# Performance work log

Hardware: AMD Instinct MI355X
Metric: run time of the kernel (lower is better)

Reference implementation:

```python
import jax, jax.numpy as jnp
import numpy as np

N, NODE_IN, EDGE_IN, H, ROUNDS = 768, 64, 32, 128, 2


def setup_inputs() -> dict:
    key = jax.random.key(0)
    ks = jax.random.split(key, 12)
    node_feats = jax.random.normal(ks[0], (N, NODE_IN), dtype=jnp.float32)
    edge_feats = jax.random.normal(ks[1], (N, N, EDGE_IN), dtype=jnp.float32)
    adj_mask = jax.random.randint(ks[2], (N, N), 0, 2).astype(jnp.float32)
    def lin(k, fan_in, fan_out):
        w = jax.random.normal(k, (fan_in, fan_out), dtype=jnp.float32) / jnp.sqrt(fan_in)
        return w
    return {
        "node_feats": node_feats,
        "edge_feats": edge_feats,
        "adj_mask": adj_mask,
        "Wn": lin(ks[3], NODE_IN, H), "bn": jnp.zeros((H,), jnp.float32),
        "We": lin(ks[4], EDGE_IN, H), "be": jnp.zeros((H,), jnp.float32),
        "Wa": lin(ks[5], 2 * H, H), "ba": jnp.zeros((H,), jnp.float32),
        "Wu": lin(ks[6], 2 * H, H), "bu": jnp.zeros((H,), jnp.float32),
    }


def reference(node_feats, edge_feats, adj_mask, Wn, bn, We, be, Wa, ba, Wu, bu):
    relu = jax.nn.relu
    h = relu(node_feats @ Wn + bn)                      # (N, H)
    e = relu(jnp.einsum('ijf,fk->ijk', edge_feats, We) + be)  # (N, N, H)
    deg = jnp.clip(adj_mask.sum(axis=0), 1.0)[:, None]  # (N, 1) receiver degree
    # Precompute edge contribution to agg_lin once (constant across rounds):
    # concat([sender, e]) @ Wa == sender @ Wa[:H] + e @ Wa[H:]
    e_proj = jnp.einsum('ijh,hk->ijk', e, Wa[H:])       # (N, N, H)
    for _ in range(ROUNDS):
        s_proj = h @ Wa[:H]                              # (N, H) sender part
        msgs = relu(s_proj[:, None, :] + e_proj + ba)    # (N, N, H)
        agg = jnp.einsum('ijk,ij->jk', msgs, adj_mask) / deg  # masked sum over senders i
        h = relu(jnp.concatenate([h, agg], axis=-1) @ Wu + bu)
    graph_emb = h.mean(axis=0)
    return (h, graph_emb)
```

## Files before the change

### kernel.cpp

```cpp
#include <hip/hip_runtime.h>
#include <hip/hip_bf16.h>


typedef __bf16 bf16x8 __attribute__((ext_vector_type(8)));
typedef float f32x4 __attribute__((ext_vector_type(4)));

#define NN 768

static __device__ __forceinline__ unsigned short to_bf16u(float x) {
    return __builtin_bit_cast(unsigned short, (__bf16)x);
}

__global__ __launch_bounds__(256) void k_prep(
                       const float* __restrict__ adj, float* __restrict__ adjT,
                       const float* __restrict__ We, const float* __restrict__ Wa,
                       unsigned short* __restrict__ WeT, unsigned short* __restrict__ Wa2T,
                       const float* __restrict__ nf, const float* __restrict__ Wn,
                       const float* __restrict__ bn, const float* __restrict__ ba,
                       float* __restrict__ h, float* __restrict__ sp) {
    const int b = blockIdx.x, tid = threadIdx.x;
    if (b < 576) {
        __shared__ float tile[32][33];
        int bx = b % 24, by = b / 24;
        int tx = tid & 31, ty = tid >> 5;
#pragma unroll
        for (int yy = 0; yy < 32; yy += 8)
            tile[ty + yy][tx] = adj[(size_t)(by * 32 + ty + yy) * NN + bx * 32 + tx];
        __syncthreads();
#pragma unroll
        for (int yy = 0; yy < 32; yy += 8)
            adjT[(size_t)(bx * 32 + ty + yy) * NN + by * 32 + tx] = tile[tx][ty + yy];
    } else if (b < 656) {
        int g = (b - 576) * 256 + tid;
        if (g < 128 * 32) {
            int c = g >> 5, f = g & 31;
            WeT[g] = to_bf16u(We[f * 128 + c]);
        } else {
            int g2 = g - 128 * 32;
            int c = g2 >> 7, k = g2 & 127;
            Wa2T[g2] = to_bf16u(Wa[(128 + k) * 128 + c]);
        }
    } else if (b < 1040) {
        __shared__ float nf_l[2][64];
        __shared__ float h_l[2][128];
        int row = tid >> 7, t = tid & 127;
        int i = (b - 656) * 2 + row;
        if (t < 64) nf_l[row][t] = nf[i * 64 + t];
        __syncthreads();
        float acc = bn[t];
#pragma unroll 8
        for (int f = 0; f < 64; ++f) acc += nf_l[row][f] * Wn[f * 128 + t];
        acc = fmaxf(acc, 0.f);
        h[i * 128 + t] = acc;
        h_l[row][t] = acc;
        __syncthreads();
        float spv = ba[t];
#pragma unroll 8
        for (int f = 0; f < 128; ++f) spv += h_l[row][f] * Wa[f * 128 + t];
        sp[i * 128 + t] = spv;
    } else {
        if (tid < 128) sp[(size_t)NN * 128 + tid] = -1e30f;
    }
}

__global__ __launch_bounds__(512) void k_big(
    const float* __restrict__ ef, const float* __restrict__ adjT,
    const float* __restrict__ sp, const unsigned short* __restrict__ WeT,
    const unsigned short* __restrict__ Wa2T, const float* __restrict__ be,
    float* __restrict__ agg) {
    __shared__ __align__(16) unsigned short e_lds[2][2][16 * 128];
    __shared__ unsigned short idx_lds[NN];
    __shared__ float be_lds[128];
    __shared__ int s_cnt;
    __shared__ float s_invdeg;

    const int tid  = threadIdx.x;
    const int j    = blockIdx.x;
    const int lane = tid & 63;
    const int wv   = tid >> 6;
    const int wr   = wv >> 2;
    const int wc   = wv & 3;
    const int lg   = lane >> 4;
    const int lr   = lane & 15;

    if (tid < 128) be_lds[tid] = be[tid];

    bf16x8 bwe[2];
    bf16x8 bwa[2][4];
#pragma unroll
    for (int t = 0; t < 2; ++t) {
        const int col = 32 * wc + 16 * t + lr;
        bwe[t] = *reinterpret_cast<const bf16x8*>(WeT + col * 32 + 8 * lg);
#pragma unroll
        for (int s = 0; s < 4; ++s)
            bwa[t][s] = *reinterpret_cast<const bf16x8*>(Wa2T + col * 128 + 32 * s + 8 * lg);
    }

    if (wv == 0) {
        int cnt = 0;
#pragma unroll
        for (int b = 0; b < 12; ++b) {
            float v = adjT[(size_t)j * NN + b * 64 + lane];
            unsigned long long m = __ballot(v != 0.0f);
            if (v != 0.0f) {
                int pos = cnt + __popcll(m & ((1ULL << lane) - 1ULL));
                idx_lds[pos] = (unsigned short)(b * 64 + lane);
            }
            cnt += (int)__popcll(m);
        }
        if (lane == 0) {
            s_cnt = cnt;
            s_invdeg = 1.0f / fmaxf((float)cnt, 1.0f);
        }
    }
    __syncthreads();

    const int cnt = s_cnt;
    const int Kc = (cnt + 31) >> 5;

    float aggp[2] = {0.f, 0.f};

    auto load_ef = [&](int m, float4& x0, float4& x1) {
        int s = 32 * m + 16 * wr + lr;
        int r = (s < cnt) ? (int)idx_lds[s] : 0;
        const float* p = ef + ((size_t)r * NN + j) * 32 + 8 * lg;
        x0 = *reinterpret_cast<const float4*>(p);
        x1 = *reinterpret_cast<const float4*>(p + 4);
    };
    auto gemm1 = [&](const float4& x0, const float4& x1, int buf) {
        bf16x8 a;
        a[0] = (__bf16)x0.x; a[1] = (__bf16)x0.y; a[2] = (__bf16)x0.z; a[3] = (__bf16)x0.w;
        a[4] = (__bf16)x1.x; a[5] = (__bf16)x1.y; a[6] = (__bf16)x1.z; a[7] = (__bf16)x1.w;
#pragma unroll
        for (int t = 0; t < 2; ++t) {
            const int col = 32 * wc + 16 * t + lr;
            float bb = be_lds[col];
            f32x4 c;
            c[0] = bb; c[1] = bb; c[2] = bb; c[3] = bb;
            f32x4 C1 = __builtin_amdgcn_mfma_f32_16x16x32_bf16(a, bwe[t], c, 0, 0, 0);
#pragma unroll
            for (int r = 0; r < 4; ++r) {
                int row = 4 * lg + r;
                int idx = (row * 128 + col) ^ ((row & 7) << 3);
                e_lds[buf][wr][idx] = to_bf16u(fmaxf(C1[r], 0.f));
            }
        }
    };

    float4 c0, c1;
    if (Kc > 0) {
        load_ef(0, c0, c1);
        gemm1(c0, c1, 0);
        if (Kc > 1) load_ef(1, c0, c1);
    }
    __syncthreads();

    for (int n = 0; n < Kc; ++n) {
        const int b = n & 1;
        float4 p0, p1;
        if (n + 2 < Kc) load_ef(n + 2, p0, p1);
        if (n + 1 < Kc) gemm1(c0, c1, b ^ 1);

        bf16x8 ae[4];
#pragma unroll
        for (int s = 0; s < 4; ++s) {
            int idx = (lr * 128 + 32 * s + 8 * lg) ^ ((lr & 7) << 3);
            ae[s] = *reinterpret_cast<const bf16x8*>(&e_lds[b][wr][idx]);
        }
        int srow[4];
#pragma unroll
        for (int r = 0; r < 4; ++r) {
            int s = 32 * n + 16 * wr + 4 * lg + r;
            srow[r] = (s < cnt) ? (int)idx_lds[s] : NN;
        }
#pragma unroll
        for (int t = 0; t < 2; ++t) {
            const int col = 32 * wc + 16 * t + lr;
            f32x4 acc;
#pragma unroll
            for (int r = 0; r < 4; ++r)
                acc[r] = sp[(size_t)srow[r] * 128 + col];
#pragma unroll
            for (int s = 0; s < 4; ++s)
                acc = __builtin_amdgcn_mfma_f32_16x16x32_bf16(ae[s], bwa[t][s], acc, 0, 0, 0);
#pragma unroll
            for (int r = 0; r < 4; ++r)
                aggp[t] += fmaxf(acc[r], 0.f);
        }

        if (n + 2 < Kc) { c0 = p0; c1 = p1; }
        __syncthreads();
    }

    float* red = reinterpret_cast<float*>(&e_lds[0][0][0]);
#pragma unroll
    for (int t = 0; t < 2; ++t) {
        float v = aggp[t];
        v += __shfl_xor(v, 16);
        v += __shfl_xor(v, 32);
        if (lane < 16) red[wv * 32 + 16 * t + lane] = v;
    }
    __syncthreads();
    if (tid < 128) {
        int wcol = tid >> 5, c32 = tid & 31;
        agg[(size_t)j * 128 + tid] =
            (red[wcol * 32 + c32] + red[(4 + wcol) * 32 + c32]) * s_invdeg;
    }
}

template <int LAST>
__global__ __launch_bounds__(256) void k_upd(
                      const float* __restrict__ h_in, const float* __restrict__ agg,
                      const float* __restrict__ Wu, const float* __restrict__ bu,
                      const float* __restrict__ Wa, const float* __restrict__ ba,
                      float* __restrict__ h_out, float* __restrict__ sp,
                      float* __restrict__ out) {
    __shared__ float buf[2][256];
    __shared__ float hn[2][128];
    const int tid = threadIdx.x;
    const int row = tid >> 7, t = tid & 127;
    const int i = blockIdx.x * 2 + row;
    buf[row][t] = h_in[i * 128 + t];
    buf[row][128 + t] = agg[i * 128 + t];
    __syncthreads();
    float acc = bu[t];
#pragma unroll 8
    for (int f = 0; f < 256; ++f) acc += buf[row][f] * Wu[f * 128 + t];
    acc = fmaxf(acc, 0.f);
    if (LAST) {
        out[i * 128 + t] = acc;
    } else {
        h_out[i * 128 + t] = acc;
        hn[row][t] = acc;
        __syncthreads();
        float spv = ba[t];
#pragma unroll 8
        for (int f = 0; f < 128; ++f) spv += hn[row][f] * Wa[f * 128 + t];
        sp[i * 128 + t] = spv;
    }
}

__global__ __launch_bounds__(64) void k_gemb(const float* __restrict__ out_h, float* __restrict__ out) {
    int c = blockIdx.x, l = threadIdx.x;
    float acc = 0.f;
    for (int i = l; i < NN; i += 64) acc += out_h[(size_t)i * 128 + c];
#pragma unroll
    for (int off = 32; off; off >>= 1) acc += __shfl_down(acc, off);
    if (l == 0) out[NN * 128 + c] = acc * (1.0f / 768.0f);
}

extern "C" void kernel_launch(void* const* d_in, const int* in_sizes, int n_in,
                              void* d_out, int out_size, void* d_ws, size_t ws_size,
                              hipStream_t stream) {
    const float* nf  = (const float*)d_in[0];
    const float* ef  = (const float*)d_in[1];
    const float* adj = (const float*)d_in[2];
    const float* Wn  = (const float*)d_in[3];
    const float* bn  = (const float*)d_in[4];
    const float* We  = (const float*)d_in[5];
    const float* be  = (const float*)d_in[6];
    const float* Wa  = (const float*)d_in[7];
    const float* ba  = (const float*)d_in[8];
    const float* Wu  = (const float*)d_in[9];
    const float* bu  = (const float*)d_in[10];
    float* out = (float*)d_out;

    float* h_buf = (float*)d_ws;
    float* agg   = h_buf + NN * 128;
    float* sp    = agg + NN * 128;
    float* adjT  = sp + (NN + 1) * 128;
    unsigned short* WeT  = (unsigned short*)(adjT + NN * NN);
    unsigned short* Wa2T = WeT + 128 * 32;

    k_prep<<<1041, 256, 0, stream>>>(adj, adjT, We, Wa, WeT, Wa2T, nf, Wn, bn, ba, h_buf, sp);

    k_big<<<NN, 512, 0, stream>>>(ef, adjT, sp, WeT, Wa2T, be, agg);
    k_upd<0><<<NN / 2, 256, 0, stream>>>(h_buf, agg, Wu, bu, Wa, ba, h_buf, sp, out);
    k_big<<<NN, 512, 0, stream>>>(ef, adjT, sp, WeT, Wa2T, be, agg);
    k_upd<1><<<NN / 2, 256, 0, stream>>>(h_buf, agg, Wu, bu, Wa, ba, h_buf, sp, out);

    k_gemb<<<128, 64, 0, stream>>>(out, out);
}
```

Measured before the change: 146.0 us.

## Pre-transpose edge features to bf16 receiver-major layout for gather kernel

Adds a transpose kernel that converts edge features to bf16 laid out as [receiver][sender][feature]. A new aggregation kernel then reads contiguous, half-size rows per receiver in both rounds. The aim is to cut the strided fp32 gather traffic in the message kernel. The cost is an extra full pass over the edge tensor plus a large workspace write. The new path is used only when the workspace is big enough.

```diff
diff --git a/kernel.cpp b/kernel.cpp
--- a/kernel.cpp
+++ b/kernel.cpp
@@ -60,6 +60,171 @@
         sp[i * 128 + t] = spv;
     } else {
         if (tid < 128) sp[(size_t)NN * 128 + tid] = -1e30f;
+    }
+}
+
+__global__ __launch_bounds__(256) void k_eft(const float* __restrict__ ef,
+                                             unsigned short* __restrict__ efT) {
+    __shared__ unsigned short tile[8 * 1288 + 8];
+    const int b = blockIdx.x, t = threadIdx.x;
+    const int i0 = (b % 24) * 32, j0 = (b / 24) * 8;
+    {
+        const int jj = t >> 5, ff = t & 31;
+#pragma unroll 4
+        for (int i = 0; i < 32; ++i) {
+            float v = ef[((size_t)(i0 + i) * NN + j0 + jj) * 32 + ff];
+            tile[jj * 1288 + i * 40 + ff] = to_bf16u(v);
+        }
+    }
+    __syncthreads();
+    const int tp = t & 31, j = t >> 5;
+    unsigned short* dst = efT + ((size_t)(j0 + j) * NN + i0) * 32;
+#pragma unroll
+    for (int v = 0; v < 4; ++v) {
+        int flat = v * 256 + tp * 8;
+        int i = flat >> 5, f = flat & 31;
+        bf16x8 val = *reinterpret_cast<const bf16x8*>(&tile[j * 1288 + i * 40 + f]);
+        *reinterpret_cast<bf16x8*>(dst + flat) = val;
+    }
+}
+
+__global__ __launch_bounds__(512) void k_big_t(
+    const unsigned short* __restrict__ efT, const float* __restrict__ adjT,
+    const float* __restrict__ sp, const unsigned short* __restrict__ WeT,
+    const unsigned short* __restrict__ Wa2T, const float* __restrict__ be,
+    float* __restrict__ agg) {
+    __shared__ __align__(16) unsigned short e_lds[2][2][16 * 128];
+    __shared__ unsigned short idx_lds[NN];
+    __shared__ float be_lds[128];
+    __shared__ int s_cnt;
+    __shared__ float s_invdeg;
+
+    const int tid  = threadIdx.x;
+    const int j    = blockIdx.x;
+    const int lane = tid & 63;
+    const int wv   = tid >> 6;
+    const int wr   = wv >> 2;
+    const int wc   = wv & 3;
+    const int lg   = lane >> 4;
+    const int lr   = lane & 15;
+
+    if (tid < 128) be_lds[tid] = be[tid];
+
+    bf16x8 bwe[2];
+    bf16x8 bwa[2][4];
+#pragma unroll
+    for (int t = 0; t < 2; ++t) {
+        const int col = 32 * wc + 16 * t + lr;
+        bwe[t] = *reinterpret_cast<const bf16x8*>(WeT + col * 32 + 8 * lg);
+#pragma unroll
+        for (int s = 0; s < 4; ++s)
+            bwa[t][s] = *reinterpret_cast<const bf16x8*>(Wa2T + col * 128 + 32 * s + 8 * lg);
+    }
+
+    if (wv == 0) {
+        int cnt = 0;
+#pragma unroll
+        for (int b = 0; b < 12; ++b) {
+            float v = adjT[(size_t)j * NN + b * 64 + lane];
+            unsigned long long m = __ballot(v != 0.0f);
+            if (v != 0.0f) {
+                int pos = cnt + __popcll(m & ((1ULL << lane) - 1ULL));
+                idx_lds[pos] = (unsigned short)(b * 64 + lane);
+            }
+            cnt += (int)__popcll(m);
+        }
+        if (lane == 0) {
+            s_cnt = cnt;
+            s_invdeg = 1.0f / fmaxf((float)cnt, 1.0f);
+        }
+    }
+    __syncthreads();
+
+    const int cnt = s_cnt;
+    const int Kc = (cnt + 31) >> 5;
+
+    float aggp[2] = {0.f, 0.f};
+
+    auto load_ef = [&](int m, bf16x8& x) {
+        int s = 32 * m + 16 * wr + lr;
+        int r = (s < cnt) ? (int)idx_lds[s] : 0;
+        x = *reinterpret_cast<const bf16x8*>(efT + ((size_t)j * NN + r) * 32 + 8 * lg);
+    };
+    auto gemm1 = [&](bf16x8 a, int buf) {
+#pragma unroll
+        for (int t = 0; t < 2; ++t) {
+            const int col = 32 * wc + 16 * t + lr;
+            float bb = be_lds[col];
+            f32x4 c;
+            c[0] = bb; c[1] = bb; c[2] = bb; c[3] = bb;
+            f32x4 C1 = __builtin_amdgcn_mfma_f32_16x16x32_bf16(a, bwe[t], c, 0, 0, 0);
+#pragma unroll
+            for (int r = 0; r < 4; ++r) {
+                int row = 4 * lg + r;
+                int idx = (row * 128 + col) ^ ((row & 7) << 3);
+                e_lds[buf][wr][idx] = to_bf16u(fmaxf(C1[r], 0.f));
+            }
+        }
+    };
+
+    bf16x8 cA;
+    if (Kc > 0) {
+        load_ef(0, cA);
+        gemm1(cA, 0);
+        if (Kc > 1) load_ef(1, cA);
+    }
+    __syncthreads();
+
+    for (int n = 0; n < Kc; ++n) {
+        const int b = n & 1;
+        bf16x8 pA;
+        if (n + 2 < Kc) load_ef(n + 2, pA);
+        if (n + 1 < Kc) gemm1(cA, b ^ 1);
+
+        bf16x8 ae[4];
+#pragma unroll
+        for (int s = 0; s < 4; ++s) {
+            int idx = (lr * 128 + 32 * s + 8 * lg) ^ ((lr & 7) << 3);
+            ae[s] = *reinterpret_cast<const bf16x8*>(&e_lds[b][wr][idx]);
+        }
+        int srow[4];
+#pragma unroll
+        for (int r = 0; r < 4; ++r) {
+            int s = 32 * n + 16 * wr + 4 * lg + r;
+            srow[r] = (s < cnt) ? (int)idx_lds[s] : NN;
+        }
+#pragma unroll
+        for (int t = 0; t < 2; ++t) {
+            const int col = 32 * wc + 16 * t + lr;
+            f32x4 acc;
+#pragma unroll
+            for (int r = 0; r < 4; ++r)
+                acc[r] = sp[(size_t)srow[r] * 128 + col];
+#pragma unroll
+            for (int s = 0; s < 4; ++s)
+                acc = __builtin_amdgcn_mfma_f32_16x16x32_bf16(ae[s], bwa[t][s], acc, 0, 0, 0);
+#pragma unroll
+            for (int r = 0; r < 4; ++r)
+                aggp[t] += fmaxf(acc[r], 0.f);
+        }
+
+        if (n + 2 < Kc) cA = pA;
+        __syncthreads();
+    }
+
+    float* red = reinterpret_cast<float*>(&e_lds[0][0][0]);
+#pragma unroll
+    for (int t = 0; t < 2; ++t) {
+        float v = aggp[t];
+        v += __shfl_xor(v, 16);
+        v += __shfl_xor(v, 32);
+        if (lane < 16) red[wv * 32 + 16 * t + lane] = v;
+    }
+    __syncthreads();
+    if (tid < 128) {
+        int wcol = tid >> 5, c32 = tid & 31;
+        agg[(size_t)j * 128 + tid] =
+            (red[wcol * 32 + c32] + red[(4 + wcol) * 32 + c32]) * s_invdeg;
     }
 }
 
@@ -271,13 +436,27 @@
     float* adjT  = sp + (NN + 1) * 128;
     unsigned short* WeT  = (unsigned short*)(adjT + NN * NN);
     unsigned short* Wa2T = WeT + 128 * 32;
+    unsigned short* efT  = Wa2T + 128 * 128;
+
+    const size_t need = (size_t)(NN * 128 * 2 + (NN + 1) * 128 + NN * NN) * 4
+                      + (size_t)(128 * 32 + 128 * 128) * 2
+                      + (size_t)NN * NN * 32 * 2;
+    const bool use_t = ws_size >= need;
 
     k_prep<<<1041, 256, 0, stream>>>(adj, adjT, We, Wa, WeT, Wa2T, nf, Wn, bn, ba, h_buf, sp);
 
-    k_big<<<NN, 512, 0, stream>>>(ef, adjT, sp, WeT, Wa2T, be, agg);
-    k_upd<0><<<NN / 2, 256, 0, stream>>>(h_buf, agg, Wu, bu, Wa, ba, h_buf, sp, out);
-    k_big<<<NN, 512, 0, stream>>>(ef, adjT, sp, WeT, Wa2T, be, agg);
-    k_upd<1><<<NN / 2, 256, 0, stream>>>(h_buf, agg, Wu, bu, Wa, ba, h_buf, sp, out);
+    if (use_t) {
+        k_eft<<<24 * 96, 256, 0, stream>>>(ef, efT);
+        k_big_t<<<NN, 512, 0, stream>>>(efT, adjT, sp, WeT, Wa2T, be, agg);
+        k_upd<0><<<NN / 2, 256, 0, stream>>>(h_buf, agg, Wu, bu, Wa, ba, h_buf, sp, out);
+        k_big_t<<<NN, 512, 0, stream>>>(efT, adjT, sp, WeT, Wa2T, be, agg);
+        k_upd<1><<<NN / 2, 256, 0, stream>>>(h_buf, agg, Wu, bu, Wa, ba, h_buf, sp, out);
+    } else {
+        k_big<<<NN, 512, 0, stream>>>(ef, adjT, sp, WeT, Wa2T, be, agg);
+        k_upd<0><<<NN / 2, 256, 0, stream>>>(h_buf, agg, Wu, bu, Wa, ba, h_buf, sp, out);
+        k_big<<<NN, 512, 0, stream>>>(ef, adjT, sp, WeT, Wa2T, be, agg);
+        k_upd<1><<<NN / 2, 256, 0, stream>>>(h_buf, agg, Wu, bu, Wa, ba, h_buf, sp, out);
+    }
 
     k_gemb<<<128, 64, 0, stream>>>(out, out);
 }
```

New measurement: 140.0 us. 1.04x faster.

## Pre-transpose edge features to bf16 receiver-major layout and process all senders densely

Applied to the files above, without the earlier changes.

The prep kernel now transposes edge_feats once into a bf16 [j][i][f] array, so each receiver block in the main kernel reads contiguous rows instead of gathering strided fp32 sender rows. The sparse compaction of neighbours is replaced by a dense loop over all 768 senders, with the adjacency value multiplied into the ReLU output. This makes the edge reads coalesced and halves their size, but roughly doubles the MFMA work for a half-dense mask. It also adds an extra full pass over the 75MB edge tensor in the prep kernel.

```diff
diff --git a/kernel.cpp b/kernel.cpp
--- a/kernel.cpp
+++ b/kernel.cpp
@@ -12,6 +12,7 @@
 }
 
 __global__ __launch_bounds__(256) void k_prep(
+                       const float* __restrict__ ef, unsigned short* __restrict__ efT,
                        const float* __restrict__ adj, float* __restrict__ adjT,
                        const float* __restrict__ We, const float* __restrict__ Wa,
                        unsigned short* __restrict__ WeT, unsigned short* __restrict__ Wa2T,
@@ -19,9 +20,31 @@
                        const float* __restrict__ bn, const float* __restrict__ ba,
                        float* __restrict__ h, float* __restrict__ sp) {
     const int b = blockIdx.x, tid = threadIdx.x;
-    if (b < 576) {
+    if (b < 2304) {
+        __shared__ unsigned short tile[8 * 1288 + 8];
+        const int i0 = (b % 24) * 32, j0 = (b / 24) * 8;
+        {
+            const int jj = tid >> 5, ff = tid & 31;
+#pragma unroll 4
+            for (int i = 0; i < 32; ++i) {
+                float v = ef[((size_t)(i0 + i) * NN + j0 + jj) * 32 + ff];
+                tile[jj * 1288 + i * 40 + ff] = to_bf16u(v);
+            }
+        }
+        __syncthreads();
+        const int tp = tid & 31, j = tid >> 5;
+        unsigned short* dst = efT + ((size_t)(j0 + j) * NN + i0) * 32;
+#pragma unroll
+        for (int v = 0; v < 4; ++v) {
+            int flat = v * 256 + tp * 8;
+            int i = flat >> 5, f = flat & 31;
+            bf16x8 val = *reinterpret_cast<const bf16x8*>(&tile[j * 1288 + i * 40 + f]);
+            *reinterpret_cast<bf16x8*>(dst + flat) = val;
+        }
+    } else if (b < 2880) {
         __shared__ float tile[32][33];
-        int bx = b % 24, by = b / 24;
+        int bb = b - 2304;
+        int bx = bb % 24, by = bb / 24;
         int tx = tid & 31, ty = tid >> 5;
 #pragma unroll
         for (int yy = 0; yy < 32; yy += 8)
@@ -30,8 +53,8 @@
 #pragma unroll
         for (int yy = 0; yy < 32; yy += 8)
             adjT[(size_t)(bx * 32 + ty + yy) * NN + by * 32 + tx] = tile[tx][ty + yy];
-    } else if (b < 656) {
-        int g = (b - 576) * 256 + tid;
+    } else if (b < 2960) {
+        int g = (b - 2880) * 256 + tid;
         if (g < 128 * 32) {
             int c = g >> 5, f = g & 31;
             WeT[g] = to_bf16u(We[f * 128 + c]);
@@ -40,11 +63,11 @@
             int c = g2 >> 7, k = g2 & 127;
             Wa2T[g2] = to_bf16u(Wa[(128 + k) * 128 + c]);
         }
-    } else if (b < 1040) {
+    } else {
         __shared__ float nf_l[2][64];
         __shared__ float h_l[2][128];
         int row = tid >> 7, t = tid & 127;
-        int i = (b - 656) * 2 + row;
+        int i = (b - 2960) * 2 + row;
         if (t < 64) nf_l[row][t] = nf[i * 64 + t];
         __syncthreads();
         float acc = bn[t];
@@ -58,20 +81,18 @@
 #pragma unroll 8
         for (int f = 0; f < 128; ++f) spv += h_l[row][f] * Wa[f * 128 + t];
         sp[i * 128 + t] = spv;
-    } else {
-        if (tid < 128) sp[(size_t)NN * 128 + tid] = -1e30f;
-    }
-}
-
-__global__ __launch_bounds__(512) void k_big(
-    const float* __restrict__ ef, const float* __restrict__ adjT,
+    }
+}
+
+__global__ __launch_bounds__(512) void k_big_s(
+    const unsigned short* __restrict__ efT, const float* __restrict__ adjT,
     const float* __restrict__ sp, const unsigned short* __restrict__ WeT,
     const unsigned short* __restrict__ Wa2T, const float* __restrict__ be,
     float* __restrict__ agg) {
     __shared__ __align__(16) unsigned short e_lds[2][2][16 * 128];
-    __shared__ unsigned short idx_lds[NN];
+    __shared__ float adj_lds[NN];
     __shared__ float be_lds[128];
-    __shared__ int s_cnt;
+    __shared__ float wred[8];
     __shared__ float s_invdeg;
 
     const int tid  = threadIdx.x;
@@ -83,6 +104,15 @@
     const int lg   = lane >> 4;
     const int lr   = lane & 15;
 
+    float asum = 0.f;
+    for (int k = tid; k < NN; k += 512) {
+        float a = adjT[(size_t)j * NN + k];
+        adj_lds[k] = a;
+        asum += a;
+    }
+#pragma unroll
+    for (int off = 32; off; off >>= 1) asum += __shfl_down(asum, off);
+    if (lane == 0) wred[wv] = asum;
     if (tid < 128) be_lds[tid] = be[tid];
 
     bf16x8 bwe[2];
@@ -95,42 +125,21 @@
         for (int s = 0; s < 4; ++s)
             bwa[t][s] = *reinterpret_cast<const bf16x8*>(Wa2T + col * 128 + 32 * s + 8 * lg);
     }
-
-    if (wv == 0) {
-        int cnt = 0;
-#pragma unroll
-        for (int b = 0; b < 12; ++b) {
-            float v = adjT[(size_t)j * NN + b * 64 + lane];
-            unsigned long long m = __ballot(v != 0.0f);
-            if (v != 0.0f) {
-                int pos = cnt + __popcll(m & ((1ULL << lane) - 1ULL));
-                idx_lds[pos] = (unsigned short)(b * 64 + lane);
-            }
-            cnt += (int)__popcll(m);
-        }
-        if (lane == 0) {
-            s_cnt = cnt;
-            s_invdeg = 1.0f / fmaxf((float)cnt, 1.0f);
-        }
-    }
-    __syncthreads();
-
-    const int cnt = s_cnt;
-    const int Kc = (cnt + 31) >> 5;
+    __syncthreads();
+    if (tid == 0) {
+        float d = 0.f;
+#pragma unroll
+        for (int w = 0; w < 8; ++w) d += wred[w];
+        s_invdeg = 1.0f / fmaxf(d, 1.0f);
+    }
 
     float aggp[2] = {0.f, 0.f};
 
-    auto load_ef = [&](int m, float4& x0, float4& x1) {
-        int s = 32 * m + 16 * wr + lr;
-        int r = (s < cnt) ? (int)idx_lds[s] : 0;
-        const float* p = ef + ((size_t)r * NN + j) * 32 + 8 * lg;
-        x0 = *reinterpret_cast<const float4*>(p);
-        x1 = *reinterpret_cast<const float4*>(p + 4);
+    auto load_ef = [&](int n, bf16x8& x) {
+        int row = 32 * n + 16 * wr + lr;
+        x = *reinterpret_cast<const bf16x8*>(efT + ((size_t)j * NN + row) * 32 + 8 * lg);
     };
-    auto gemm1 = [&](const float4& x0, const float4& x1, int buf) {
-        bf16x8 a;
-        a[0] = (__bf16)x0.x; a[1] = (__bf16)x0.y; a[2] = (__bf16)x0.z; a[3] = (__bf16)x0.w;
-        a[4] = (__bf16)x1.x; a[5] = (__bf16)x1.y; a[6] = (__bf16)x1.z; a[7] = (__bf16)x1.w;
+    auto gemm1 = [&](bf16x8 a, int buf) {
 #pragma unroll
         for (int t = 0; t < 2; ++t) {
             const int col = 32 * wc + 16 * t + lr;
@@ -147,19 +156,17 @@
         }
     };
 
-    float4 c0, c1;
-    if (Kc > 0) {
-        load_ef(0, c0, c1);
-        gemm1(c0, c1, 0);
-        if (Kc > 1) load_ef(1, c0, c1);
-    }
-    __syncthreads();
-
-    for (int n = 0; n < Kc; ++n) {
+    bf16x8 cA;
+    load_ef(0, cA);
+    gemm1(cA, 0);
+    load_ef(1, cA);
+    __syncthreads();
+
+    for (int n = 0; n < 24; ++n) {
         const int b = n & 1;
-        float4 p0, p1;
-        if (n + 2 < Kc) load_ef(n + 2, p0, p1);
-        if (n + 1 < Kc) gemm1(c0, c1, b ^ 1);
+        bf16x8 pA;
+        if (n + 2 < 24) load_ef(n + 2, pA);
+        if (n + 1 < 24) gemm1(cA, b ^ 1);
 
         bf16x8 ae[4];
 #pragma unroll
@@ -167,28 +174,24 @@
             int idx = (lr * 128 + 32 * s + 8 * lg) ^ ((lr & 7) << 3);
             ae[s] = *reinterpret_cast<const bf16x8*>(&e_lds[b][wr][idx]);
         }
-        int srow[4];
-#pragma unroll
-        for (int r = 0; r < 4; ++r) {
-            int s = 32 * n + 16 * wr + 4 * lg + r;
-            srow[r] = (s < cnt) ? (int)idx_lds[s] : NN;
-        }
+        const int i0 = 32 * n + 16 * wr + 4 * lg;
+        f32x4 av = *reinterpret_cast<const f32x4*>(&adj_lds[i0]);
 #pragma unroll
         for (int t = 0; t < 2; ++t) {
             const int col = 32 * wc + 16 * t + lr;
             f32x4 acc;
 #pragma unroll
             for (int r = 0; r < 4; ++r)
-                acc[r] = sp[(size_t)srow[r] * 128 + col];
+                acc[r] = sp[(size_t)(i0 + r) * 128 + col];
 #pragma unroll
             for (int s = 0; s < 4; ++s)
                 acc = __builtin_amdgcn_mfma_f32_16x16x32_bf16(ae[s], bwa[t][s], acc, 0, 0, 0);
 #pragma unroll
             for (int r = 0; r < 4; ++r)
-                aggp[t] += fmaxf(acc[r], 0.f);
-        }
-
-        if (n + 2 < Kc) { c0 = p0; c1 = p1; }
+                aggp[t] += fmaxf(acc[r], 0.f) * av[r];
+        }
+
+        if (n + 2 < 24) cA = pA;
         __syncthreads();
     }
 
@@ -271,12 +274,14 @@
     float* adjT  = sp + (NN + 1) * 128;
     unsigned short* WeT  = (unsigned short*)(adjT + NN * NN);
     unsigned short* Wa2T = WeT + 128 * 32;
-
-    k_prep<<<1041, 256, 0, stream>>>(adj, adjT, We, Wa, WeT, Wa2T, nf, Wn, bn, ba, h_buf, sp);
-
-    k_big<<<NN, 512, 0, stream>>>(ef, adjT, sp, WeT, Wa2T, be, agg);
+    unsigned short* efT  = Wa2T + 128 * 128;
+
+    k_prep<<<3344, 256, 0, stream>>>(ef, efT, adj, adjT, We, Wa, WeT, Wa2T,
+                                     nf, Wn, bn, ba, h_buf, sp);
+
+    k_big_s<<<NN, 512, 0, stream>>>(efT, adjT, sp, WeT, Wa2T, be, agg);
     k_upd<0><<<NN / 2, 256, 0, stream>>>(h_buf, agg, Wu, bu, Wa, ba, h_buf, sp, out);
-    k_big<<<NN, 512, 0, stream>>>(ef, adjT, sp, WeT, Wa2T, be, agg);
+    k_big_s<<<NN, 512, 0, stream>>>(efT, adjT, sp, WeT, Wa2T, be, agg);
     k_upd<1><<<NN / 2, 256, 0, stream>>>(h_buf, agg, Wu, bu, Wa, ba, h_buf, sp, out);
 
     k_gemb<<<128, 64, 0, stream>>>(out, out);
```

New measurement: 139.8 us. 4.2% less time.

## Materialize edge projection once in bf16 and stream it densely each round

Applied to the files above, without the earlier changes.

Adds a k_build kernel that computes the full N×N×H edge projection once (edge MLP then Wa2 GEMM via MFMA) and stores it in global memory as bf16. Each round then runs a simple streaming kernel that adds the sender projection, applies relu, masks by adj and writes per-segment partial sums. k_upd reduces those partials and scales by a degree inverse that k_prep now computes. This removes the per-round recomputation of both GEMMs and the adjacency compaction. In exchange it writes and rereads a roughly 150 MB intermediate and no longer skips masked senders, and the projection is rounded to bf16 before the relu.

```diff
diff --git a/kernel.cpp b/kernel.cpp
--- a/kernel.cpp
+++ b/kernel.cpp
@@ -12,26 +12,16 @@
 }
 
 __global__ __launch_bounds__(256) void k_prep(
-                       const float* __restrict__ adj, float* __restrict__ adjT,
+                       const float* __restrict__ adj,
                        const float* __restrict__ We, const float* __restrict__ Wa,
                        unsigned short* __restrict__ WeT, unsigned short* __restrict__ Wa2T,
                        const float* __restrict__ nf, const float* __restrict__ Wn,
                        const float* __restrict__ bn, const float* __restrict__ ba,
-                       float* __restrict__ h, float* __restrict__ sp) {
+                       float* __restrict__ h, float* __restrict__ sp,
+                       float* __restrict__ invdeg) {
     const int b = blockIdx.x, tid = threadIdx.x;
-    if (b < 576) {
-        __shared__ float tile[32][33];
-        int bx = b % 24, by = b / 24;
-        int tx = tid & 31, ty = tid >> 5;
-#pragma unroll
-        for (int yy = 0; yy < 32; yy += 8)
-            tile[ty + yy][tx] = adj[(size_t)(by * 32 + ty + yy) * NN + bx * 32 + tx];
-        __syncthreads();
-#pragma unroll
-        for (int yy = 0; yy < 32; yy += 8)
-            adjT[(size_t)(bx * 32 + ty + yy) * NN + by * 32 + tx] = tile[tx][ty + yy];
-    } else if (b < 656) {
-        int g = (b - 576) * 256 + tid;
+    if (b < 80) {
+        int g = b * 256 + tid;
         if (g < 128 * 32) {
             int c = g >> 5, f = g & 31;
             WeT[g] = to_bf16u(We[f * 128 + c]);
@@ -40,11 +30,11 @@
             int c = g2 >> 7, k = g2 & 127;
             Wa2T[g2] = to_bf16u(Wa[(128 + k) * 128 + c]);
         }
-    } else if (b < 1040) {
+    } else if (b < 464) {
         __shared__ float nf_l[2][64];
         __shared__ float h_l[2][128];
         int row = tid >> 7, t = tid & 127;
-        int i = (b - 656) * 2 + row;
+        int i = (b - 80) * 2 + row;
         if (t < 64) nf_l[row][t] = nf[i * 64 + t];
         __syncthreads();
         float acc = bn[t];
@@ -59,23 +49,30 @@
         for (int f = 0; f < 128; ++f) spv += h_l[row][f] * Wa[f * 128 + t];
         sp[i * 128 + t] = spv;
     } else {
-        if (tid < 128) sp[(size_t)NN * 128 + tid] = -1e30f;
-    }
-}
-
-__global__ __launch_bounds__(512) void k_big(
-    const float* __restrict__ ef, const float* __restrict__ adjT,
-    const float* __restrict__ sp, const unsigned short* __restrict__ WeT,
+        __shared__ float dsum[4][64];
+        int d = b - 464;
+        int q = tid >> 6, jj = tid & 63;
+        int j = d * 64 + jj;
+        float s = 0.f;
+        for (int i = q * 192; i < q * 192 + 192; ++i)
+            s += adj[(size_t)i * NN + j];
+        dsum[q][jj] = s;
+        __syncthreads();
+        if (tid < 64) {
+            float tot = dsum[0][tid] + dsum[1][tid] + dsum[2][tid] + dsum[3][tid];
+            invdeg[d * 64 + tid] = 1.0f / fmaxf(tot, 1.0f);
+        }
+    }
+}
+
+__global__ __launch_bounds__(512) void k_build(
+    const float* __restrict__ ef, const unsigned short* __restrict__ WeT,
     const unsigned short* __restrict__ Wa2T, const float* __restrict__ be,
-    float* __restrict__ agg) {
-    __shared__ __align__(16) unsigned short e_lds[2][2][16 * 128];
-    __shared__ unsigned short idx_lds[NN];
-    __shared__ float be_lds[128];
-    __shared__ int s_cnt;
-    __shared__ float s_invdeg;
-
+    unsigned short* __restrict__ eproj) {
+    __shared__ unsigned short ef_lds[128 * 40];
+    __shared__ __align__(16) unsigned short e_lds[128 * 128];
     const int tid  = threadIdx.x;
-    const int j    = blockIdx.x;
+    const size_t g0 = (size_t)blockIdx.x * 128;
     const int lane = tid & 63;
     const int wv   = tid >> 6;
     const int wr   = wv >> 2;
@@ -83,134 +80,158 @@
     const int lg   = lane >> 4;
     const int lr   = lane & 15;
 
-    if (tid < 128) be_lds[tid] = be[tid];
-
+    {
+        int row = tid >> 2, c0 = (tid & 3) * 8;
+        const float* src = ef + (g0 + row) * 32 + c0;
+        float4 f0 = *reinterpret_cast<const float4*>(src);
+        float4 f1 = *reinterpret_cast<const float4*>(src + 4);
+        bf16x8 v;
+        v[0] = (__bf16)f0.x; v[1] = (__bf16)f0.y; v[2] = (__bf16)f0.z; v[3] = (__bf16)f0.w;
+        v[4] = (__bf16)f1.x; v[5] = (__bf16)f1.y; v[6] = (__bf16)f1.z; v[7] = (__bf16)f1.w;
+        *reinterpret_cast<bf16x8*>(&ef_lds[row * 40 + c0]) = v;
+    }
     bf16x8 bwe[2];
     bf16x8 bwa[2][4];
+    float bereg[2];
 #pragma unroll
     for (int t = 0; t < 2; ++t) {
         const int col = 32 * wc + 16 * t + lr;
         bwe[t] = *reinterpret_cast<const bf16x8*>(WeT + col * 32 + 8 * lg);
+        bereg[t] = be[col];
 #pragma unroll
         for (int s = 0; s < 4; ++s)
             bwa[t][s] = *reinterpret_cast<const bf16x8*>(Wa2T + col * 128 + 32 * s + 8 * lg);
     }
-
-    if (wv == 0) {
-        int cnt = 0;
-#pragma unroll
-        for (int b = 0; b < 12; ++b) {
-            float v = adjT[(size_t)j * NN + b * 64 + lane];
-            unsigned long long m = __ballot(v != 0.0f);
-            if (v != 0.0f) {
-                int pos = cnt + __popcll(m & ((1ULL << lane) - 1ULL));
-                idx_lds[pos] = (unsigned short)(b * 64 + lane);
-            }
-            cnt += (int)__popcll(m);
-        }
-        if (lane == 0) {
-            s_cnt = cnt;
-            s_invdeg = 1.0f / fmaxf((float)cnt, 1.0f);
-        }
-    }
-    __syncthreads();
-
-    const int cnt = s_cnt;
-    const int Kc = (cnt + 31) >> 5;
-
-    float aggp[2] = {0.f, 0.f};
-
-    auto load_ef = [&](int m, float4& x0, float4& x1) {
-        int s = 32 * m + 16 * wr + lr;
-        int r = (s < cnt) ? (int)idx_lds[s] : 0;
-        const float* p = ef + ((size_t)r * NN + j) * 32 + 8 * lg;
-        x0 = *reinterpret_cast<const float4*>(p);
-        x1 = *reinterpret_cast<const float4*>(p + 4);
-    };
-    auto gemm1 = [&](const float4& x0, const float4& x1, int buf) {
-        bf16x8 a;
-        a[0] = (__bf16)x0.x; a[1] = (__bf16)x0.y; a[2] = (__bf16)x0.z; a[3] = (__bf16)x0.w;
-        a[4] = (__bf16)x1.x; a[5] = (__bf16)x1.y; a[6] = (__bf16)x1.z; a[7] = (__bf16)x1.w;
+    __syncthreads();
+
+#pragma unroll
+    for (int s = 0; s < 4; ++s) {
+        const int arow = 64 * wr + 16 * s + lr;
+        bf16x8 a = *reinterpret_cast<const bf16x8*>(&ef_lds[arow * 40 + 8 * lg]);
 #pragma unroll
         for (int t = 0; t < 2; ++t) {
             const int col = 32 * wc + 16 * t + lr;
-            float bb = be_lds[col];
             f32x4 c;
-            c[0] = bb; c[1] = bb; c[2] = bb; c[3] = bb;
+            c[0] = bereg[t]; c[1] = bereg[t]; c[2] = bereg[t]; c[3] = bereg[t];
             f32x4 C1 = __builtin_amdgcn_mfma_f32_16x16x32_bf16(a, bwe[t], c, 0, 0, 0);
 #pragma unroll
             for (int r = 0; r < 4; ++r) {
-                int row = 4 * lg + r;
+                int row = 64 * wr + 16 * s + 4 * lg + r;
                 int idx = (row * 128 + col) ^ ((row & 7) << 3);
-                e_lds[buf][wr][idx] = to_bf16u(fmaxf(C1[r], 0.f));
+                e_lds[idx] = to_bf16u(fmaxf(C1[r], 0.f));
             }
         }
-    };
-
-    float4 c0, c1;
-    if (Kc > 0) {
-        load_ef(0, c0, c1);
-        gemm1(c0, c1, 0);
-        if (Kc > 1) load_ef(1, c0, c1);
-    }
-    __syncthreads();
-
-    for (int n = 0; n < Kc; ++n) {
-        const int b = n & 1;
-        float4 p0, p1;
-        if (n + 2 < Kc) load_ef(n + 2, p0, p1);
-        if (n + 1 < Kc) gemm1(c0, c1, b ^ 1);
-
+    }
+    __syncthreads();
+
+    ushort4 outv[4][2];
+#pragma unroll
+    for (int s = 0; s < 4; ++s) {
+        const int arow = 64 * wr + 16 * s + lr;
         bf16x8 ae[4];
 #pragma unroll
-        for (int s = 0; s < 4; ++s) {
-            int idx = (lr * 128 + 32 * s + 8 * lg) ^ ((lr & 7) << 3);
-            ae[s] = *reinterpret_cast<const bf16x8*>(&e_lds[b][wr][idx]);
-        }
-        int srow[4];
-#pragma unroll
-        for (int r = 0; r < 4; ++r) {
-            int s = 32 * n + 16 * wr + 4 * lg + r;
-            srow[r] = (s < cnt) ? (int)idx_lds[s] : NN;
-        }
+        for (int ss = 0; ss < 4; ++ss) {
+            int idx = (arow * 128 + 32 * ss + 8 * lg) ^ ((arow & 7) << 3);
+            ae[ss] = *reinterpret_cast<const bf16x8*>(&e_lds[idx]);
+        }
+#pragma unroll
+        for (int t = 0; t < 2; ++t) {
+            f32x4 acc;
+            acc[0] = 0.f; acc[1] = 0.f; acc[2] = 0.f; acc[3] = 0.f;
+#pragma unroll
+            for (int ss = 0; ss < 4; ++ss)
+                acc = __builtin_amdgcn_mfma_f32_16x16x32_bf16(ae[ss], bwa[t][ss], acc, 0, 0, 0);
+            outv[s][t].x = to_bf16u(acc[0]);
+            outv[s][t].y = to_bf16u(acc[1]);
+            outv[s][t].z = to_bf16u(acc[2]);
+            outv[s][t].w = to_bf16u(acc[3]);
+        }
+    }
+    __syncthreads();
+
+#pragma unroll
+    for (int s = 0; s < 4; ++s)
 #pragma unroll
         for (int t = 0; t < 2; ++t) {
             const int col = 32 * wc + 16 * t + lr;
-            f32x4 acc;
-#pragma unroll
-            for (int r = 0; r < 4; ++r)
-                acc[r] = sp[(size_t)srow[r] * 128 + col];
-#pragma unroll
-            for (int s = 0; s < 4; ++s)
-                acc = __builtin_amdgcn_mfma_f32_16x16x32_bf16(ae[s], bwa[t][s], acc, 0, 0, 0);
-#pragma unroll
-            for (int r = 0; r < 4; ++r)
-                aggp[t] += fmaxf(acc[r], 0.f);
-        }
-
-        if (n + 2 < Kc) { c0 = p0; c1 = p1; }
-        __syncthreads();
-    }
-
-    float* red = reinterpret_cast<float*>(&e_lds[0][0][0]);
-#pragma unroll
-    for (int t = 0; t < 2; ++t) {
-        float v = aggp[t];
-        v += __shfl_xor(v, 16);
-        v += __shfl_xor(v, 32);
-        if (lane < 16) red[wv * 32 + 16 * t + lane] = v;
-    }
-    __syncthreads();
-    if (tid < 128) {
-        int wcol = tid >> 5, c32 = tid & 31;
-        agg[(size_t)j * 128 + tid] =
-            (red[wcol * 32 + c32] + red[(4 + wcol) * 32 + c32]) * s_invdeg;
-    }
+#pragma unroll
+            for (int r = 0; r < 4; ++r) {
+                int row = 64 * wr + 16 * s + 4 * lg + r;
+                int idx = (row * 128 + col) ^ ((row & 7) << 3);
+                unsigned short val = (r == 0) ? outv[s][t].x : (r == 1) ? outv[s][t].y
+                                   : (r == 2) ? outv[s][t].z : outv[s][t].w;
+                e_lds[idx] = val;
+            }
+        }
+    __syncthreads();
+
+    {
+        int row = tid >> 2;
+#pragma unroll
+        for (int m = 0; m < 4; ++m) {
+            int a = (tid & 3) + 4 * m;
+            int idx = row * 128 + 8 * (a ^ (row & 7));
+            f32x4 v = *reinterpret_cast<const f32x4*>(&e_lds[idx]);
+            *reinterpret_cast<f32x4*>(eproj + (g0 + row) * 128 + 8 * a) = v;
+        }
+    }
+}
+
+__global__ __launch_bounds__(256) void k_round(
+    const unsigned short* __restrict__ eproj, const float* __restrict__ adj,
+    const float* __restrict__ sp, float* __restrict__ aggp) {
+    const int tid = threadIdx.x;
+    const int jt  = blockIdx.x >> 4;
+    const int seg = blockIdx.x & 15;
+    const int j0  = jt * 16;
+    const int i0  = seg * 48;
+    const int jj  = tid >> 4;
+    const int kb  = (tid & 15) * 8;
+
+    const size_t estep = (size_t)NN * 128;
+    const unsigned short* ep = eproj + ((size_t)i0 * NN + j0 + jj) * 128 + kb;
+    const float* ap = adj + (size_t)i0 * NN + j0 + jj;
+    const float* spp = sp + (size_t)i0 * 128 + kb;
+
+    float acc[8] = {0.f, 0.f, 0.f, 0.f, 0.f, 0.f, 0.f, 0.f};
+
+    bf16x8 v = *reinterpret_cast<const bf16x8*>(ep);
+    float av = *ap;
+    float4 s0 = *reinterpret_cast<const float4*>(spp);
+    float4 s1 = *reinterpret_cast<const float4*>(spp + 4);
+
+    for (int m = 0; m < 48; ++m) {
+        bf16x8 vn = v; float avn = av; float4 s0n = s0, s1n = s1;
+        if (m < 47) {
+            vn = *reinterpret_cast<const bf16x8*>(ep + estep);
+            avn = ap[NN];
+            s0n = *reinterpret_cast<const float4*>(spp + 128);
+            s1n = *reinterpret_cast<const float4*>(spp + 132);
+        }
+        acc[0] += fmaxf(s0.x + (float)v[0], 0.f) * av;
+        acc[1] += fmaxf(s0.y + (float)v[1], 0.f) * av;
+        acc[2] += fmaxf(s0.z + (float)v[2], 0.f) * av;
+        acc[3] += fmaxf(s0.w + (float)v[3], 0.f) * av;
+        acc[4] += fmaxf(s1.x + (float)v[4], 0.f) * av;
+        acc[5] += fmaxf(s1.y + (float)v[5], 0.f) * av;
+        acc[6] += fmaxf(s1.z + (float)v[6], 0.f) * av;
+        acc[7] += fmaxf(s1.w + (float)v[7], 0.f) * av;
+        ep += estep; ap += NN; spp += 128;
+        v = vn; av = avn; s0 = s0n; s1 = s1n;
+    }
+
+    float* dst = aggp + ((size_t)(j0 + jj) * 16 + seg) * 128 + kb;
+    float4 o0, o1;
+    o0.x = acc[0]; o0.y = acc[1]; o0.z = acc[2]; o0.w = acc[3];
+    o1.x = acc[4]; o1.y = acc[5]; o1.z = acc[6]; o1.w = acc[7];
+    *reinterpret_cast<float4*>(dst) = o0;
+    *reinterpret_cast<float4*>(dst + 4) = o1;
 }
 
 template <int LAST>
 __global__ __launch_bounds__(256) void k_upd(
-                      const float* __restrict__ h_in, const float* __restrict__ agg,
+                      const float* __restrict__ h_in, const float* __restrict__ aggp,
+                      const float* __restrict__ invdeg,
                       const float* __restrict__ Wu, const float* __restrict__ bu,
                       const float* __restrict__ Wa, const float* __restrict__ ba,
                       float* __restrict__ h_out, float* __restrict__ sp,
@@ -219,24 +240,28 @@
     __shared__ float hn[2][128];
     const int tid = threadIdx.x;
     const int row = tid >> 7, t = tid & 127;
-    const int i = blockIdx.x * 2 + row;
-    buf[row][t] = h_in[i * 128 + t];
-    buf[row][128 + t] = agg[i * 128 + t];
+    const int j = blockIdx.x * 2 + row;
+    float s = 0.f;
+#pragma unroll
+    for (int seg = 0; seg < 16; ++seg)
+        s += aggp[((size_t)j * 16 + seg) * 128 + t];
+    buf[row][t] = h_in[j * 128 + t];
+    buf[row][128 + t] = s * invdeg[j];
     __syncthreads();
     float acc = bu[t];
 #pragma unroll 8
     for (int f = 0; f < 256; ++f) acc += buf[row][f] * Wu[f * 128 + t];
     acc = fmaxf(acc, 0.f);
     if (LAST) {
-        out[i * 128 + t] = acc;
+        out[j * 128 + t] = acc;
     } else {
-        h_out[i * 128 + t] = acc;
+        h_out[j * 128 + t] = acc;
         hn[row][t] = acc;
         __syncthreads();
         float spv = ba[t];
 #pragma unroll 8
         for (int f = 0; f < 128; ++f) spv += hn[row][f] * Wa[f * 128 + t];
-        sp[i * 128 + t] = spv;
+        sp[j * 128 + t] = spv;
     }
 }
 
@@ -265,19 +290,22 @@
     const float* bu  = (const float*)d_in[10];
     float* out = (float*)d_out;
 
-    float* h_buf = (float*)d_ws;
-    float* agg   = h_buf + NN * 128;
-    float* sp    = agg + NN * 128;
-    float* adjT  = sp + (NN + 1) * 128;
-    unsigned short* WeT  = (unsigned short*)(adjT + NN * NN);
-    unsigned short* Wa2T = WeT + 128 * 32;
-
-    k_prep<<<1041, 256, 0, stream>>>(adj, adjT, We, Wa, WeT, Wa2T, nf, Wn, bn, ba, h_buf, sp);
-
-    k_big<<<NN, 512, 0, stream>>>(ef, adjT, sp, WeT, Wa2T, be, agg);
-    k_upd<0><<<NN / 2, 256, 0, stream>>>(h_buf, agg, Wu, bu, Wa, ba, h_buf, sp, out);
-    k_big<<<NN, 512, 0, stream>>>(ef, adjT, sp, WeT, Wa2T, be, agg);
-    k_upd<1><<<NN / 2, 256, 0, stream>>>(h_buf, agg, Wu, bu, Wa, ba, h_buf, sp, out);
+    float* h_buf  = (float*)d_ws;
+    float* sp     = h_buf + NN * 128;
+    float* invdeg = sp + NN * 128;
+    float* aggp   = invdeg + NN;
+    unsigned short* WeT   = (unsigned short*)(aggp + (size_t)NN * 16 * 128);
+    unsigned short* Wa2T  = WeT + 128 * 32;
+    unsigned short* eproj = Wa2T + 128 * 128;
+
+    k_prep<<<476, 256, 0, stream>>>(adj, We, Wa, WeT, Wa2T, nf, Wn, bn, ba,
+                                    h_buf, sp, invdeg);
+    k_build<<<NN * NN / 128, 512, 0, stream>>>(ef, WeT, Wa2T, be, eproj);
+
+    k_round<<<48 * 16, 256, 0, stream>>>(eproj, adj, sp, aggp);
+    k_upd<0><<<NN / 2, 256, 0, stream>>>(h_buf, aggp, invdeg, Wu, bu, Wa, ba, h_buf, sp, out);
+    k_round<<<48 * 16, 256, 0, stream>>>(eproj, adj, sp, aggp);
+    k_upd<1><<<NN / 2, 256, 0, stream>>>(h_buf, aggp, invdeg, Wu, bu, Wa, ba, h_buf, sp, out);
 
     k_gemb<<<128, 64, 0, stream>>>(out, out);
 }
```

After: 152.6 us. 1.05x slower.
